# Kernel tuning notes

Measured on AMD Instinct MI355X. Metric: run time of the kernel, lower is better.

Reference implementation:

```python
import jax, jax.numpy as jnp
import numpy as np

# db4 analysis filters (pywt convention); synthesis reuses same filters (orthogonal wavelet,
# correlation analysis + convolution synthesis gives perfect reconstruction under periodization).
DEC_LO = [-0.010597401784997278, 0.032883011666982945, 0.030841381835986965, -0.18703481171888114,
          -0.02798376941698385, 0.6308807679295904, 0.7148465705525415, 0.23037781330885523]
DEC_HI = [-0.23037781330885523, 0.7148465705525415, -0.6308807679295904, -0.02798376941698385,
          0.18703481171888114, 0.030841381835986965, -0.032883011666982945, -0.010597401784997278]
LEVELS = 3

def _analysis(x, filt):
    # a[n] = sum_k filt[k] * x[(2n+k) mod L]  (circular filter + downsample-by-2)
    y = sum(c * jnp.roll(x, -k, axis=-1) for k, c in enumerate(filt))
    return y[..., ::2]

def _synthesis(a, filt):
    # upsample-by-2 (zeros at odd positions) then circular convolution with filt
    u = jnp.zeros(a.shape[:-1] + (2 * a.shape[-1],), a.dtype).at[..., ::2].set(a)
    return sum(c * jnp.roll(u, k, axis=-1) for k, c in enumerate(filt))

def _decompose(z, levels):
    details, cur = [], z
    for _ in range(levels):
        details.append(_analysis(cur, DEC_HI))
        cur = _analysis(cur, DEC_LO)
    return cur, details

def _reconstruct(approx, details):
    cur = approx
    for d in reversed(details):
        cur = _synthesis(cur, DEC_LO) + _synthesis(d, DEC_HI)
    return cur

def _soft_threshold(c, lam_raw):
    # dynamic per-(batch,channel) threshold scaled by learnable softplus(lam_raw)
    lam = jax.nn.softplus(lam_raw) * jnp.mean(jnp.abs(c), axis=-1)  # [B,H]
    thr = jnp.sign(c) * jnp.maximum(jnp.abs(c) - lam[..., None], 0.0)
    return thr, lam

def _film(c, flow_raw, Wgb, bgb, Wg, bg):
    # FiLM gamma/beta from flow features, sigmoid-gated
    gb = flow_raw @ Wgb.T + bgb                      # [B, 2H]
    H = c.shape[1]
    gamma, beta = gb[:, :H], gb[:, H:]
    gate = jax.nn.sigmoid(flow_raw @ Wg + bg)[:, None, None]  # [B,1,1]
    return c * (1.0 + gate * gamma[:, :, None]) + gate * beta[:, :, None]

def setup_inputs() -> dict:
    key = jax.random.key(0)
    ks = jax.random.split(key, 8)
    B, L, C, Hd = 16, 4096, 64, 128
    x = jax.random.normal(ks[0], (B, L, C), jnp.float32)
    mask = jnp.ones((B, L), jnp.float32)
    flow_raw = jax.random.normal(ks[1], (B, 24), jnp.float32)
    W_in = jax.random.normal(ks[2], (Hd, C), jnp.float32) / np.sqrt(C)
    b_in = jnp.zeros((Hd,), jnp.float32)
    W_mix = jax.random.normal(ks[3], (Hd, Hd), jnp.float32) / np.sqrt(Hd)
    b_mix = jnp.zeros((Hd,), jnp.float32)
    lam_raw = jnp.full((LEVELS + 1,), 0.5413248538970947, jnp.float32)  # softplus^-1(1.0)
    film_Wgb = jax.random.normal(ks[4], (LEVELS + 1, 2 * Hd, 24), jnp.float32) * 0.05
    film_bgb = jnp.zeros((LEVELS + 1, 2 * Hd), jnp.float32)
    film_Wg = jax.random.normal(ks[5], (LEVELS + 1, 24), jnp.float32) * 0.05
    film_bg = jnp.zeros((LEVELS + 1,), jnp.float32)
    return dict(x=x, mask=mask, flow_raw=flow_raw, W_in=W_in, b_in=b_in, W_mix=W_mix, b_mix=b_mix,
                lam_raw=lam_raw, film_Wgb=film_Wgb, film_bgb=film_bgb, film_Wg=film_Wg, film_bg=film_bg)

def reference(x, mask, flow_raw, W_in, b_in, W_mix, b_mix, lam_raw, film_Wgb, film_bgb, film_Wg, film_bg):
    xp = x.transpose(0, 2, 1) * mask[:, None, :]               # [B,C,L]
    z = jnp.einsum('hc,bcl->bhl', W_in, xp) + b_in[:, None]    # input_proj (1x1 conv)
    approx, details = _decompose(z, LEVELS)
    approx = _film(approx, flow_raw, film_Wgb[0], film_bgb[0], film_Wg[0], film_bg[0])
    details = [_film(d, flow_raw, film_Wgb[i + 1], film_bgb[i + 1], film_Wg[i + 1], film_bg[i + 1])
               for i, d in enumerate(details)]
    approx_t, lam_a = _soft_threshold(approx, lam_raw[0])
    dts, lams = [], [lam_a]
    for i, d in enumerate(details):
        dt, lam_d = _soft_threshold(d, lam_raw[i + 1])
        dts.append(dt)
        lams.append(lam_d)
    z_rec = _reconstruct(approx_t, dts)
    mixed = jnp.einsum('gh,bhl->bgl', W_mix, z + z_rec) + b_mix[:, None]  # mix (1x1 conv)
    out = jax.nn.gelu(mixed, approximate=False)                 # torch nn.GELU is exact
    h_seq = out.transpose(0, 2, 1) * mask[..., None]            # [B,L,H]
    denom = jnp.clip(jnp.sum(mask, axis=1, keepdims=True), 1.0, None)
    h_pool = jnp.sum(h_seq * mask[..., None], axis=1) / denom   # masked mean pool [B,H]
    lam_cat = jnp.concatenate([l.reshape(l.shape[0], -1) for l in lams], axis=1)
    return h_seq, h_pool, jnp.mean(lam_cat, axis=1), jnp.max(lam_cat, axis=1)
```

## Files before the change

kernel.cpp:

```cpp
#include <hip/hip_runtime.h>
#include <math.h>

#define BB 16
#define LL 4096
#define CC 64
#define HD 128

typedef __attribute__((ext_vector_type(8))) short short8;
typedef __attribute__((ext_vector_type(8))) unsigned short ushort8;
typedef __attribute__((ext_vector_type(4))) float floatx4;

__constant__ float c_lo[8] = {
    -0.010597401784997278f, 0.032883011666982945f, 0.030841381835986965f,
    -0.18703481171888114f, -0.02798376941698385f, 0.6308807679295904f,
    0.7148465705525415f, 0.23037781330885523f};
__constant__ float c_hi[8] = {
    -0.23037781330885523f, 0.7148465705525415f, -0.6308807679295904f,
    -0.02798376941698385f, 0.18703481171888114f, 0.030841381835986965f,
    -0.032883011666982945f, -0.010597401784997278f};

__device__ __forceinline__ float gelu_exact(float x) {
    return 0.5f * x * (1.0f + erff(x * 0.70710678118654752440f));
}
__device__ __forceinline__ unsigned short f2b(float f) {
    unsigned int u = __float_as_uint(f);
    u = u + 0x7FFFu + ((u >> 16) & 1u);
    return (unsigned short)(u >> 16);
}
__device__ __forceinline__ float b2f(unsigned short s) {
    return __uint_as_float(((unsigned int)s) << 16);
}


__global__ __launch_bounds__(256) void zproj_kernel(
    const float* __restrict__ x, const float* __restrict__ mask,
    const float* __restrict__ W_in, const float* __restrict__ b_in,
    unsigned short* __restrict__ z_bf,
    const float* __restrict__ W_mix, unsigned short* __restrict__ Bmix,
    const float* __restrict__ flow, const float* __restrict__ Wgb,
    const float* __restrict__ bgb, const float* __restrict__ Wg,
    const float* __restrict__ bg, float* __restrict__ film_ws,
    float* __restrict__ gate_ws) {
    int blk = blockIdx.x;
    int tid = threadIdx.x;

    if (blk >= BB * 64) {
        int e = blk - BB * 64;
        if (e < 64) {
            int q = e * 256 + tid;
            int g = (q >> 3) & 127;
            int h = ((q >> 10) << 3) | (q & 7);
            Bmix[q] = f2b(W_mix[g * HD + h]);
        } else {
            int bf = e - 64;
            int f = bf & 3;
            int b = bf >> 2;
            const float* fl = flow + b * 24;
            const float* wrow = Wgb + ((size_t)(f * 256 + tid)) * 24;
            float acc = bgb[f * 256 + tid];
#pragma unroll
            for (int j = 0; j < 24; ++j) acc = fmaf(wrow[j], fl[j], acc);
            film_ws[(size_t)bf * 256 + tid] = acc;
            if (tid == 0) {
                float g = bg[f];
#pragma unroll
                for (int j = 0; j < 24; ++j) g = fmaf(Wg[f * 24 + j], fl[j], g);
                gate_ws[bf] = 1.0f / (1.0f + expf(-g));
            }
        }
        return;
    }

    int b = blk >> 6;
    int l0 = (blk & 63) << 6;
    int lane = tid & 63;
    int w = tid >> 6;
    int h_half = w >> 1;
    int l_q = w & 1;
    int ln15 = lane & 15, lq4 = lane >> 4;

    int lr0 = l0 + l_q * 32 + ln15;
    int lr1 = lr0 + 16;
    float mk0 = mask[(size_t)b * LL + lr0];
    float mk1 = mask[(size_t)b * LL + lr1];

    floatx4 acc[4][2];
#pragma unroll
    for (int i = 0; i < 4; ++i)
#pragma unroll
        for (int j = 0; j < 2; ++j) acc[i][j] = (floatx4){0.f, 0.f, 0.f, 0.f};

#pragma unroll
    for (int ks = 0; ks < 2; ++ks) {
        int c0 = ks * 32 + (lq4 << 3);
        short8 bf0, bf1;
        {
            const float* xp = x + ((size_t)b * LL + lr0) * CC + c0;
            float4 xa = *(const float4*)xp;
            float4 xb = *(const float4*)(xp + 4);
            bf0[0] = (short)f2b(xa.x * mk0); bf0[1] = (short)f2b(xa.y * mk0);
            bf0[2] = (short)f2b(xa.z * mk0); bf0[3] = (short)f2b(xa.w * mk0);
            bf0[4] = (short)f2b(xb.x * mk0); bf0[5] = (short)f2b(xb.y * mk0);
            bf0[6] = (short)f2b(xb.z * mk0); bf0[7] = (short)f2b(xb.w * mk0);
        }
        {
            const float* xp = x + ((size_t)b * LL + lr1) * CC + c0;
            float4 xa = *(const float4*)xp;
            float4 xb = *(const float4*)(xp + 4);
            bf1[0] = (short)f2b(xa.x * mk1); bf1[1] = (short)f2b(xa.y * mk1);
            bf1[2] = (short)f2b(xa.z * mk1); bf1[3] = (short)f2b(xa.w * mk1);
            bf1[4] = (short)f2b(xb.x * mk1); bf1[5] = (short)f2b(xb.y * mk1);
            bf1[6] = (short)f2b(xb.z * mk1); bf1[7] = (short)f2b(xb.w * mk1);
        }
        int c8 = ks * 32 + (lq4 << 3);
        const float* wb = W_in + (size_t)(h_half * 64 + ln15) * CC + c8;
#pragma unroll
        for (int ht = 0; ht < 4; ++ht) {
            const float* wr = wb + (size_t)ht * 16 * CC;
            float4 wa = *(const float4*)wr;
            float4 wc = *(const float4*)(wr + 4);
            short8 af;
            af[0] = (short)f2b(wa.x); af[1] = (short)f2b(wa.y);
            af[2] = (short)f2b(wa.z); af[3] = (short)f2b(wa.w);
            af[4] = (short)f2b(wc.x); af[5] = (short)f2b(wc.y);
            af[6] = (short)f2b(wc.z); af[7] = (short)f2b(wc.w);
            acc[ht][0] = __builtin_amdgcn_mfma_f32_16x16x32_bf16(af, bf0, acc[ht][0], 0, 0, 0);
            acc[ht][1] = __builtin_amdgcn_mfma_f32_16x16x32_bf16(af, bf1, acc[ht][1], 0, 0, 0);
        }
    }

#pragma unroll
    for (int ht = 0; ht < 4; ++ht) {
#pragma unroll
        for (int r = 0; r < 4; ++r) {
            int h = h_half * 64 + ht * 16 + (lq4 << 2) + r;
            float bi = b_in[h];
            z_bf[((size_t)(b * HD + h)) * LL + lr0] = f2b(acc[ht][0][r] + bi);
            z_bf[((size_t)(b * HD + h)) * LL + lr1] = f2b(acc[ht][1][r] + bi);
        }
    }
}


__device__ __forceinline__ void analysis_step(const float* __restrict__ src,
                                              float* __restrict__ lo_dst,
                                              float* __restrict__ hi_dst,
                                              int half, int tid) {
    int len = half << 1;
    for (int q = tid; q < (half >> 2); q += 256) {
        int n0 = q << 2;
        float lo[4], hi[4];
        if (n0 + 4 == half) {
#pragma unroll
            for (int i = 0; i < 4; ++i) {
                float l = 0.f, hh = 0.f;
#pragma unroll
                for (int k = 0; k < 8; ++k) {
                    float v = src[(2 * (n0 + i) + k) & (len - 1)];
                    l = fmaf(c_lo[k], v, l);
                    hh = fmaf(c_hi[k], v, hh);
                }
                lo[i] = l; hi[i] = hh;
            }
        } else {
            float sv[16];
            const float* sp = src + (n0 << 1);
            *(float4*)&sv[0]  = *(const float4*)(sp);
            *(float4*)&sv[4]  = *(const float4*)(sp + 4);
            *(float4*)&sv[8]  = *(const float4*)(sp + 8);
            *(float4*)&sv[12] = *(const float4*)(sp + 12);
#pragma unroll
            for (int i = 0; i < 4; ++i) {
                float l = 0.f, hh = 0.f;
#pragma unroll
                for (int k = 0; k < 8; ++k) {
                    l = fmaf(c_lo[k], sv[2 * i + k], l);
                    hh = fmaf(c_hi[k], sv[2 * i + k], hh);
                }
                lo[i] = l; hi[i] = hh;
            }
        }
        *(float4*)&lo_dst[n0] = make_float4(lo[0], lo[1], lo[2], lo[3]);
        *(float4*)&hi_dst[n0] = make_float4(hi[0], hi[1], hi[2], hi[3]);
    }
}

__device__ __forceinline__ void synth_oct(const float* __restrict__ A,
                                          const float* __restrict__ D,
                                          int m0, int half, float* ov) {
    if (m0 == 0) {
        int mask2 = (half << 1) - 1;
#pragma unroll
        for (int t = 0; t < 8; ++t) {
            int par = t & 1;
            float s = 0.f;
#pragma unroll
            for (int j = 0; j < 4; ++j) {
                int k = 2 * j + par;
                int idx = ((t - k) & mask2) >> 1;
                s = fmaf(c_lo[k], A[idx], s);
                s = fmaf(c_hi[k], D[idx], s);
            }
            ov[t] = s;
        }
    } else {
        float av[8], dv[8];
        *(float4*)&av[0] = *(const float4*)(A + m0 - 4);
        *(float4*)&av[4] = *(const float4*)(A + m0);
        *(float4*)&dv[0] = *(const float4*)(D + m0 - 4);
        *(float4*)&dv[4] = *(const float4*)(D + m0);
#pragma unroll
        for (int t = 0; t < 4; ++t) {
            float e = 0.f, o = 0.f;
#pragma unroll
            for (int j = 0; j < 4; ++j) {
                float xa = av[t + 4 - j], xd = dv[t + 4 - j];
                e = fmaf(c_lo[2 * j], xa, e);     e = fmaf(c_hi[2 * j], xd, e);
                o = fmaf(c_lo[2 * j + 1], xa, o); o = fmaf(c_hi[2 * j + 1], xd, o);
            }
            ov[2 * t] = e;
            ov[2 * t + 1] = o;
        }
    }
}

__device__ __forceinline__ void synth_step(const float* __restrict__ A,
                                           const float* __restrict__ D,
                                           float* __restrict__ dst,
                                           int half, int tid) {
    for (int q = tid; q < (half >> 2); q += 256) {
        int m0 = q << 2;
        int i0 = m0 << 1;
        float ov[8];
        synth_oct(A, D, m0, half, ov);
        *(float4*)&dst[i0]     = make_float4(ov[0], ov[1], ov[2], ov[3]);
        *(float4*)&dst[i0 + 4] = make_float4(ov[4], ov[5], ov[6], ov[7]);
    }
}


__global__ __launch_bounds__(256) void wavelet_kernel(const unsigned short* __restrict__ z_bf,
                                                      unsigned short* __restrict__ s_bf,
                                                      const float* __restrict__ film_ws,
                                                      const float* __restrict__ gate_ws,
                                                      const float* __restrict__ lam_raw,
                                                      float* __restrict__ lam_ws) {
    __shared__ float zrow[4096];
    __shared__ float d1[2048];
    __shared__ float d2[1024];
    __shared__ float Aq[2048];
    __shared__ float Bq[1024];

    int blk = blockIdx.x;
    int b = blk >> 7;
    int h = blk & 127;
    int tid = threadIdx.x;
    const unsigned short* zg = z_bf + ((size_t)(b * HD + h)) * LL;
    unsigned short* sg = s_bf + ((size_t)(b * HD + h)) * LL;

    for (int i = tid; i < 512; i += 256) {
        ushort8 v = *(const ushort8*)(zg + (i << 3));
        *(float4*)&zrow[i << 3] =
            make_float4(b2f(v[0]), b2f(v[1]), b2f(v[2]), b2f(v[3]));
        *(float4*)&zrow[(i << 3) + 4] =
            make_float4(b2f(v[4]), b2f(v[5]), b2f(v[6]), b2f(v[7]));
    }
    __syncthreads();

    analysis_step(zrow, Aq, d1, 2048, tid);
    __syncthreads();
    analysis_step(Aq, Bq, d2, 1024, tid);
    __syncthreads();
    analysis_step(Bq, Aq, Aq + 512, 512, tid);
    __syncthreads();

    float sc0, sh0, sc1, sh1, sc2, sh2, sc3, sh3;
    {
        int base = b * 4;
#define FILM_COEF(bd, SC, SH)                                              \
        {   float ga = film_ws[((size_t)(base + bd)) * 256 + h];           \
            float be = film_ws[((size_t)(base + bd)) * 256 + 128 + h];     \
            float gt = gate_ws[base + bd];                                 \
            SC = 1.0f + gt * ga; SH = gt * be; }
        FILM_COEF(0, sc0, sh0) FILM_COEF(1, sc1, sh1)
        FILM_COEF(2, sc2, sh2) FILM_COEF(3, sc3, sh3)
#undef FILM_COEF
    }
    float s0 = 0.f, s1 = 0.f, s2 = 0.f, s3 = 0.f;
#define FILM4(P, LEN, SC, SH, SUM)                                         \
    for (int qq = tid; qq < ((LEN) >> 2); qq += 256) {                     \
        float4 v = *(float4*)&(P)[qq << 2];                                \
        v.x = fmaf(v.x, SC, SH); v.y = fmaf(v.y, SC, SH);                  \
        v.z = fmaf(v.z, SC, SH); v.w = fmaf(v.w, SC, SH);                  \
        *(float4*)&(P)[qq << 2] = v;                                       \
        SUM += fabsf(v.x) + fabsf(v.y) + fabsf(v.z) + fabsf(v.w);          \
    }
    FILM4(Aq, 512, sc0, sh0, s0)
    FILM4(d1, 2048, sc1, sh1, s1)
    FILM4(d2, 1024, sc2, sh2, s2)
    FILM4((Aq + 512), 512, sc3, sh3, s3)
#undef FILM4
#pragma unroll
    for (int off = 32; off > 0; off >>= 1) {
        s0 += __shfl_xor(s0, off);
        s1 += __shfl_xor(s1, off);
        s2 += __shfl_xor(s2, off);
        s3 += __shfl_xor(s3, off);
    }
    if ((tid & 63) == 0)
        ((float4*)Bq)[tid >> 6] = make_float4(s0, s1, s2, s3);
    __syncthreads();
    float4 r0 = ((const float4*)Bq)[0];
    float4 r1 = ((const float4*)Bq)[1];
    float4 r2 = ((const float4*)Bq)[2];
    float4 r3 = ((const float4*)Bq)[3];
    float lam0 = log1pf(expf(lam_raw[0])) * ((r0.x + r1.x + r2.x + r3.x) * (1.0f / 512.f));
    float lam1 = log1pf(expf(lam_raw[1])) * ((r0.y + r1.y + r2.y + r3.y) * (1.0f / 2048.f));
    float lam2 = log1pf(expf(lam_raw[2])) * ((r0.z + r1.z + r2.z + r3.z) * (1.0f / 1024.f));
    float lam3 = log1pf(expf(lam_raw[3])) * ((r0.w + r1.w + r2.w + r3.w) * (1.0f / 512.f));
    if (tid < 4) {
        float lam = (tid == 0) ? lam0 : (tid == 1) ? lam1 : (tid == 2) ? lam2 : lam3;
        lam_ws[((size_t)(b * 4 + tid)) * 128 + h] = lam;
    }
#define STHR4(P, LEN, LAM)                                                 \
    for (int qq = tid; qq < ((LEN) >> 2); qq += 256) {                     \
        float4 v = *(float4*)&(P)[qq << 2];                                \
        float a;                                                           \
        a = fabsf(v.x) - (LAM); v.x = (a > 0.f) ? copysignf(a, v.x) : 0.f; \
        a = fabsf(v.y) - (LAM); v.y = (a > 0.f) ? copysignf(a, v.y) : 0.f; \
        a = fabsf(v.z) - (LAM); v.z = (a > 0.f) ? copysignf(a, v.z) : 0.f; \
        a = fabsf(v.w) - (LAM); v.w = (a > 0.f) ? copysignf(a, v.w) : 0.f; \
        *(float4*)&(P)[qq << 2] = v;                                       \
    }
    STHR4(Aq, 512, lam0)
    STHR4(d1, 2048, lam1)
    STHR4(d2, 1024, lam2)
    STHR4((Aq + 512), 512, lam3)
#undef STHR4
    __syncthreads();

    synth_step(Aq, Aq + 512, Bq, 512, tid);
    __syncthreads();
    synth_step(Bq, d2, Aq, 1024, tid);
    __syncthreads();
    for (int q = tid; q < 512; q += 256) {
        int m0 = q << 2;
        int i0 = m0 << 1;
        float ov[8];
        synth_oct(Aq, d1, m0, 2048, ov);
        float zr[8];
        *(float4*)&zr[0] = *(float4*)&zrow[i0];
        *(float4*)&zr[4] = *(float4*)&zrow[i0 + 4];
        ushort8 o8;
#pragma unroll
        for (int t = 0; t < 8; ++t) o8[t] = f2b(ov[t] + zr[t]);
        *(ushort8*)(sg + i0) = o8;
    }
}


union U32x4S8 { unsigned int u[4]; short8 s; };

__global__ __launch_bounds__(256) void mix_kernel(const unsigned short* __restrict__ s_bf,
                                                  const unsigned short* __restrict__ Bmix,
                                                  const float* __restrict__ b_mix,
                                                  const float* __restrict__ mask,
                                                  float* __restrict__ out,
                                                  float* __restrict__ pool_part) {
    __shared__ unsigned int T[HD * 32];
    __shared__ float pbuf[2][HD];

    int blk = blockIdx.x;
    int b = blk >> 6;
    int lt64 = blk & 63;
    int l0 = lt64 << 6;
    int tid = threadIdx.x;
    int lane = tid & 63;
    int w = tid >> 6;
    int l_half = w >> 1, g_half = w & 1;
    int ln15 = lane & 15, lq4 = lane >> 4;

    {
        const unsigned int* src = (const unsigned int*)s_bf;
#pragma unroll
        for (int r = 0; r < 4; ++r) {
            int q = (r << 8) + tid;
            int hh = q >> 3;
            int k = q & 7;
            uint4 v = *(const uint4*)(src + (size_t)(b * HD + hh) * (LL / 2) +
                                      (l0 >> 1) + (k << 2));
            int sw = hh & 31;
            unsigned int* tp = T + hh * 32;
            tp[((k << 2) + 0) ^ sw] = v.x;
            tp[((k << 2) + 1) ^ sw] = v.y;
            tp[((k << 2) + 2) ^ sw] = v.z;
            tp[((k << 2) + 3) ^ sw] = v.w;
        }
    }
    __syncthreads();

    floatx4 acc[2][4];
#pragma unroll
    for (int i = 0; i < 2; ++i)
#pragma unroll
        for (int j = 0; j < 4; ++j) acc[i][j] = (floatx4){0.f, 0.f, 0.f, 0.f};

    const unsigned short* Bb = Bmix + (g_half * 64 + ln15) * 8;

#pragma unroll 2
    for (int ks = 0; ks < 4; ++ks) {
        int koct = ks * 4 + lq4;
        short8 a[2], bb[4];
#pragma unroll
        for (int lt = 0; lt < 2; ++lt) {
            int l_loc = l_half * 32 + lt * 16 + ln15;
            int lp = l_loc >> 1;
            int odd = l_loc & 1;
            U32x4S8 cv;
#pragma unroll
            for (int qq = 0; qq < 4; ++qq) {
                int h0 = koct * 8 + 2 * qq;
                unsigned int w0 = T[h0 * 32 + (lp ^ (h0 & 31))];
                unsigned int w1 = T[(h0 + 1) * 32 + (lp ^ ((h0 + 1) & 31))];
                unsigned int e0 = odd ? (w0 >> 16) : (w0 & 0xffffu);
                unsigned int e1 = odd ? (w1 >> 16) : (w1 & 0xffffu);
                cv.u[qq] = e0 | (e1 << 16);
            }
            a[lt] = cv.s;
        }
#pragma unroll
        for (int gt = 0; gt < 4; ++gt)
            bb[gt] = *(const short8*)(Bb + (size_t)koct * 1024 + gt * 128);
#pragma unroll
        for (int lt = 0; lt < 2; ++lt)
#pragma unroll
            for (int gt = 0; gt < 4; ++gt)
                acc[lt][gt] = __builtin_amdgcn_mfma_f32_16x16x32_bf16(a[lt], bb[gt], acc[lt][gt], 0, 0, 0);
    }

    int gcol[4]; float bmv[4]; float pacc[4];
#pragma unroll
    for (int gt = 0; gt < 4; ++gt) {
        gcol[gt] = g_half * 64 + gt * 16 + ln15;
        bmv[gt] = b_mix[gcol[gt]];
        pacc[gt] = 0.f;
    }
#pragma unroll
    for (int lt = 0; lt < 2; ++lt) {
#pragma unroll
        for (int r = 0; r < 4; ++r) {
            int l = l0 + l_half * 32 + lt * 16 + (lq4 << 2) + r;
            float mkv = mask[(size_t)b * LL + l];
            float* orow = out + ((size_t)b * LL + l) * HD;
#pragma unroll
            for (int gt = 0; gt < 4; ++gt) {
                float v = gelu_exact(acc[lt][gt][r] + bmv[gt]) * mkv;
                orow[gcol[gt]] = v;
                pacc[gt] = fmaf(v, mkv, pacc[gt]);
            }
        }
    }
#pragma unroll
    for (int gt = 0; gt < 4; ++gt) {
        pacc[gt] += __shfl_xor(pacc[gt], 16);
        pacc[gt] += __shfl_xor(pacc[gt], 32);
    }
    if (lane < 16) {
#pragma unroll
        for (int gt = 0; gt < 4; ++gt)
            pbuf[l_half][g_half * 64 + gt * 16 + lane] = pacc[gt];
    }
    __syncthreads();
    if (tid < HD)
        pool_part[((size_t)(b * 64 + lt64)) * HD + tid] = pbuf[0][tid] + pbuf[1][tid];
}


__global__ void finalize_kernel(const float* __restrict__ pool_part,
                                const float* __restrict__ mask,
                                const float* __restrict__ lam_ws,
                                float* __restrict__ d_out) {
    const size_t OUT1 = (size_t)BB * LL * HD;
    const size_t OUT2 = OUT1 + (size_t)BB * HD;
    const size_t OUT3 = OUT2 + BB;
    int b = blockIdx.x, tid = threadIdx.x;
    __shared__ float rsum[256], rmax[256];
    __shared__ float dsh;

    float ms = 0.f;
    const float4* mp = (const float4*)(mask + (size_t)b * LL);
    for (int i = tid; i < LL / 4; i += 256) {
        float4 m = mp[i];
        ms += m.x + m.y + m.z + m.w;
    }
    rsum[tid] = ms; __syncthreads();
    for (int st = 128; st > 0; st >>= 1) {
        if (tid < st) rsum[tid] += rsum[tid + st];
        __syncthreads();
    }
    if (tid == 0) dsh = fmaxf(rsum[0], 1.0f);
    __syncthreads();
    float denom = dsh;

    if (tid < 128) {
        float s = 0.f;
        for (int blk = 0; blk < 64; ++blk)
            s += pool_part[((size_t)(b * 64 + blk)) * HD + tid];
        d_out[OUT1 + (size_t)b * HD + tid] = s / denom;
    }

    float v0 = lam_ws[(size_t)b * 512 + tid];
    float v1 = lam_ws[(size_t)b * 512 + 256 + tid];
    rsum[tid] = v0 + v1;
    rmax[tid] = fmaxf(v0, v1);
    __syncthreads();
    for (int st = 128; st > 0; st >>= 1) {
        if (tid < st) {
            rsum[tid] += rsum[tid + st];
            rmax[tid] = fmaxf(rmax[tid], rmax[tid + st]);
        }
        __syncthreads();
    }
    if (tid == 0) {
        d_out[OUT2 + b] = rsum[0] / 512.0f;
        d_out[OUT3 + b] = rmax[0];
    }
}


extern "C" void kernel_launch(void* const* d_in, const int* in_sizes, int n_in,
                              void* d_out, int out_size, void* d_ws, size_t ws_size,
                              hipStream_t stream) {
    (void)in_sizes; (void)n_in; (void)out_size; (void)ws_size;
    const float* x      = (const float*)d_in[0];
    const float* mask   = (const float*)d_in[1];
    const float* flow   = (const float*)d_in[2];
    const float* W_in   = (const float*)d_in[3];
    const float* b_in   = (const float*)d_in[4];
    const float* W_mix  = (const float*)d_in[5];
    const float* b_mix  = (const float*)d_in[6];
    const float* lam_raw= (const float*)d_in[7];
    const float* Wgb    = (const float*)d_in[8];
    const float* bgb    = (const float*)d_in[9];
    const float* Wg     = (const float*)d_in[10];
    const float* bg     = (const float*)d_in[11];

    unsigned short* z_bf = (unsigned short*)d_ws;
    unsigned short* s_bf = z_bf + (size_t)BB * HD * LL;
    float* film_ws   = (float*)(s_bf + (size_t)BB * HD * LL);
    float* gate_ws   = film_ws + BB * 4 * 256;
    float* lam_ws    = gate_ws + 64;
    float* pool_part = lam_ws + BB * 4 * 128;
    unsigned short* Bmix = (unsigned short*)(pool_part + BB * 64 * HD);

    float* out = (float*)d_out;

    hipLaunchKernelGGL(zproj_kernel, dim3(BB * 64 + 128), dim3(256), 0, stream,
                       x, mask, W_in, b_in, z_bf,
                       W_mix, Bmix, flow, Wgb, bgb, Wg, bg, film_ws, gate_ws);
    hipLaunchKernelGGL(wavelet_kernel, dim3(BB * HD), dim3(256), 0, stream,
                       z_bf, s_bf, film_ws, gate_ws, lam_raw, lam_ws);
    hipLaunchKernelGGL(mix_kernel, dim3(BB * (LL / 64)), dim3(256), 0, stream,
                       s_bf, Bmix, b_mix, mask, out, pool_part);
    hipLaunchKernelGGL(finalize_kernel, dim3(BB), dim3(256), 0, stream,
                       pool_part, mask, lam_ws, out);
}
```

Before: 74.17 us.

## Keep input row packed as bf16 in LDS and fuse FiLM/threshold passes

```diff
diff --git a/kernel.cpp b/kernel.cpp
--- a/kernel.cpp
+++ b/kernel.cpp
@@ -245,7 +245,7 @@
                                                       const float* __restrict__ gate_ws,
                                                       const float* __restrict__ lam_raw,
                                                       float* __restrict__ lam_ws) {
-    __shared__ float zrow[4096];
+    __shared__ unsigned int zpk[2048];
     __shared__ float d1[2048];
     __shared__ float d2[1024];
     __shared__ float Aq[2048];
@@ -255,19 +255,48 @@
     int b = blk >> 7;
     int h = blk & 127;
     int tid = threadIdx.x;
-    const unsigned short* zg = z_bf + ((size_t)(b * HD + h)) * LL;
+    const uint4* zg4 = (const uint4*)(z_bf + ((size_t)(b * HD + h)) * LL);
     unsigned short* sg = s_bf + ((size_t)(b * HD + h)) * LL;
 
-    for (int i = tid; i < 512; i += 256) {
-        ushort8 v = *(const ushort8*)(zg + (i << 3));
-        *(float4*)&zrow[i << 3] =
-            make_float4(b2f(v[0]), b2f(v[1]), b2f(v[2]), b2f(v[3]));
-        *(float4*)&zrow[(i << 3) + 4] =
-            make_float4(b2f(v[4]), b2f(v[5]), b2f(v[6]), b2f(v[7]));
-    }
-    __syncthreads();
-
-    analysis_step(zrow, Aq, d1, 2048, tid);
+    for (int i = tid; i < 512; i += 256)
+        ((uint4*)zpk)[i] = zg4[i];
+    __syncthreads();
+
+    for (int q = tid; q < 512; q += 256) {
+        int n0 = q << 2;
+        float sv[16];
+        if (n0 == 2044) {
+#pragma unroll
+            for (int j = 0; j < 14; ++j) {
+                int idx = (2 * n0 + j) & 4095;
+                unsigned int wv = zpk[idx >> 1];
+                sv[j] = b2f((unsigned short)((idx & 1) ? (wv >> 16) : (wv & 0xffffu)));
+            }
+            sv[14] = 0.f; sv[15] = 0.f;
+        } else {
+            uint4 wa = *(const uint4*)(zpk + n0);
+            uint4 wb = *(const uint4*)(zpk + n0 + 4);
+            unsigned int ww[8] = {wa.x, wa.y, wa.z, wa.w, wb.x, wb.y, wb.z, wb.w};
+#pragma unroll
+            for (int j = 0; j < 8; ++j) {
+                sv[2 * j]     = b2f((unsigned short)(ww[j] & 0xffffu));
+                sv[2 * j + 1] = b2f((unsigned short)(ww[j] >> 16));
+            }
+        }
+        float lo[4], hi[4];
+#pragma unroll
+        for (int i = 0; i < 4; ++i) {
+            float l = 0.f, hh = 0.f;
+#pragma unroll
+            for (int k = 0; k < 8; ++k) {
+                l = fmaf(c_lo[k], sv[2 * i + k], l);
+                hh = fmaf(c_hi[k], sv[2 * i + k], hh);
+            }
+            lo[i] = l; hi[i] = hh;
+        }
+        *(float4*)&Aq[n0] = make_float4(lo[0], lo[1], lo[2], lo[3]);
+        *(float4*)&d1[n0] = make_float4(hi[0], hi[1], hi[2], hi[3]);
+    }
     __syncthreads();
     analysis_step(Aq, Bq, d2, 1024, tid);
     __syncthreads();
@@ -286,29 +315,33 @@
         FILM_COEF(2, sc2, sh2) FILM_COEF(3, sc3, sh3)
 #undef FILM_COEF
     }
-    float s0 = 0.f, s1 = 0.f, s2 = 0.f, s3 = 0.f;
-#define FILM4(P, LEN, SC, SH, SUM)                                         \
-    for (int qq = tid; qq < ((LEN) >> 2); qq += 256) {                     \
-        float4 v = *(float4*)&(P)[qq << 2];                                \
-        v.x = fmaf(v.x, SC, SH); v.y = fmaf(v.y, SC, SH);                  \
-        v.z = fmaf(v.z, SC, SH); v.w = fmaf(v.w, SC, SH);                  \
-        *(float4*)&(P)[qq << 2] = v;                                       \
-        SUM += fabsf(v.x) + fabsf(v.y) + fabsf(v.z) + fabsf(v.w);          \
-    }
-    FILM4(Aq, 512, sc0, sh0, s0)
-    FILM4(d1, 2048, sc1, sh1, s1)
-    FILM4(d2, 1024, sc2, sh2, s2)
-    FILM4((Aq + 512), 512, sc3, sh3, s3)
-#undef FILM4
+
+    float* p0 = &Aq[tid << 2];
+    float* p1 = &d1[tid << 2];
+    float* p2 = &d1[1024 + (tid << 2)];
+    float* p3 = &d2[tid << 2];
+    bool lowhalf = (tid < 128);
+    float scA = lowhalf ? sc0 : sc3, shA = lowhalf ? sh0 : sh3;
+
+    float4 f0 = *(float4*)p0, f1 = *(float4*)p1, f2v = *(float4*)p2, f3 = *(float4*)p3;
+#define FILMV(V, SC, SH)                                                   \
+    { V.x = fmaf(V.x, SC, SH); V.y = fmaf(V.y, SC, SH);                    \
+      V.z = fmaf(V.z, SC, SH); V.w = fmaf(V.w, SC, SH); }
+    FILMV(f0, scA, shA) FILMV(f1, sc1, sh1) FILMV(f2v, sc1, sh1) FILMV(f3, sc2, sh2)
+#undef FILMV
+    float sA = fabsf(f0.x) + fabsf(f0.y) + fabsf(f0.z) + fabsf(f0.w);
+    float s1 = fabsf(f1.x) + fabsf(f1.y) + fabsf(f1.z) + fabsf(f1.w)
+             + fabsf(f2v.x) + fabsf(f2v.y) + fabsf(f2v.z) + fabsf(f2v.w);
+    float s2 = fabsf(f3.x) + fabsf(f3.y) + fabsf(f3.z) + fabsf(f3.w);
 #pragma unroll
     for (int off = 32; off > 0; off >>= 1) {
-        s0 += __shfl_xor(s0, off);
+        sA += __shfl_xor(sA, off);
         s1 += __shfl_xor(s1, off);
         s2 += __shfl_xor(s2, off);
-        s3 += __shfl_xor(s3, off);
     }
     if ((tid & 63) == 0)
-        ((float4*)Bq)[tid >> 6] = make_float4(s0, s1, s2, s3);
+        ((float4*)Bq)[tid >> 6] = make_float4(lowhalf ? sA : 0.f, s1, s2,
+                                              lowhalf ? 0.f : sA);
     __syncthreads();
     float4 r0 = ((const float4*)Bq)[0];
     float4 r1 = ((const float4*)Bq)[1];
@@ -322,21 +355,16 @@
         float lam = (tid == 0) ? lam0 : (tid == 1) ? lam1 : (tid == 2) ? lam2 : lam3;
         lam_ws[((size_t)(b * 4 + tid)) * 128 + h] = lam;
     }
-#define STHR4(P, LEN, LAM)                                                 \
-    for (int qq = tid; qq < ((LEN) >> 2); qq += 256) {                     \
-        float4 v = *(float4*)&(P)[qq << 2];                                \
-        float a;                                                           \
-        a = fabsf(v.x) - (LAM); v.x = (a > 0.f) ? copysignf(a, v.x) : 0.f; \
-        a = fabsf(v.y) - (LAM); v.y = (a > 0.f) ? copysignf(a, v.y) : 0.f; \
-        a = fabsf(v.z) - (LAM); v.z = (a > 0.f) ? copysignf(a, v.z) : 0.f; \
-        a = fabsf(v.w) - (LAM); v.w = (a > 0.f) ? copysignf(a, v.w) : 0.f; \
-        *(float4*)&(P)[qq << 2] = v;                                       \
-    }
-    STHR4(Aq, 512, lam0)
-    STHR4(d1, 2048, lam1)
-    STHR4(d2, 1024, lam2)
-    STHR4((Aq + 512), 512, lam3)
-#undef STHR4
+    float lamA = lowhalf ? lam0 : lam3;
+#define THRV(V, LAM)                                                       \
+    { float a;                                                             \
+      a = fabsf(V.x) - (LAM); V.x = (a > 0.f) ? copysignf(a, V.x) : 0.f;   \
+      a = fabsf(V.y) - (LAM); V.y = (a > 0.f) ? copysignf(a, V.y) : 0.f;   \
+      a = fabsf(V.z) - (LAM); V.z = (a > 0.f) ? copysignf(a, V.z) : 0.f;   \
+      a = fabsf(V.w) - (LAM); V.w = (a > 0.f) ? copysignf(a, V.w) : 0.f; }
+    THRV(f0, lamA) THRV(f1, lam1) THRV(f2v, lam1) THRV(f3, lam2)
+#undef THRV
+    *(float4*)p0 = f0; *(float4*)p1 = f1; *(float4*)p2 = f2v; *(float4*)p3 = f3;
     __syncthreads();
 
     synth_step(Aq, Aq + 512, Bq, 512, tid);
@@ -348,12 +376,16 @@
         int i0 = m0 << 1;
         float ov[8];
         synth_oct(Aq, d1, m0, 2048, ov);
-        float zr[8];
-        *(float4*)&zr[0] = *(float4*)&zrow[i0];
-        *(float4*)&zr[4] = *(float4*)&zrow[i0 + 4];
+        uint4 zw = *(const uint4*)(zpk + (i0 >> 1));
+        unsigned int zz[4] = {zw.x, zw.y, zw.z, zw.w};
         ushort8 o8;
 #pragma unroll
-        for (int t = 0; t < 8; ++t) o8[t] = f2b(ov[t] + zr[t]);
+        for (int t2 = 0; t2 < 4; ++t2) {
+            float ze = b2f((unsigned short)(zz[t2] & 0xffffu));
+            float zo = b2f((unsigned short)(zz[t2] >> 16));
+            o8[2 * t2]     = f2b(ov[2 * t2] + ze);
+            o8[2 * t2 + 1] = f2b(ov[2 * t2 + 1] + zo);
+        }
         *(ushort8*)(sg + i0) = o8;
     }
 }
```

New measurement: 71.72 us. -3.3%, faster.
